# Optimization experiments

Measured on AMD Instinct MI355X. Metric: run time of the kernel, lower is better.

Reference implementation:

```python
import jax, jax.numpy as jnp
import numpy as np

N = 100000   # nodes
E = 1600000  # directed edges (avg degree 16)
H = 64       # MODEL_HIDDEN_CHANNELS


def setup_inputs() -> dict:
    key = jax.random.key(0)
    ks = jax.random.split(key, 6)
    x = jax.random.normal(ks[0], (N, 1), dtype=jnp.float32)
    edge_index = jax.random.randint(ks[1], (2, E), 0, N, dtype=jnp.int32)
    w1 = jax.random.normal(ks[2], (1, H), dtype=jnp.float32) * 0.5
    b1 = jnp.zeros((H,), dtype=jnp.float32)
    w2 = jax.random.normal(ks[3], (H, H), dtype=jnp.float32) * (1.0 / np.sqrt(H))
    b2 = jnp.zeros((H,), dtype=jnp.float32)
    wfc = jax.random.normal(ks[4], (H, 1), dtype=jnp.float32) * (1.0 / np.sqrt(H))
    bfc = jnp.zeros((1,), dtype=jnp.float32)
    return {"x": x, "edge_index": edge_index, "w1": w1, "b1": b1,
            "w2": w2, "b2": b2, "wfc": wfc, "bfc": bfc}


def _gcn_conv(x, src, dst, norm, W, b, n):
    # PyG GCNConv: h = x @ W, then scatter-add of norm-weighted messages at dst, + bias
    h = x @ W                                   # [n, out]
    msg = h[src] * norm[:, None]                # gather + scale, [e, out]
    agg = jax.ops.segment_sum(msg, dst, num_segments=n)
    return agg + b


def reference(x, edge_index, w1, b1, w2, b2, wfc, bfc):
    n = x.shape[0]
    # add self-loops (PyG GCNConv default)
    loops = jnp.arange(n, dtype=edge_index.dtype)
    src = jnp.concatenate([edge_index[0], loops])
    dst = jnp.concatenate([edge_index[1], loops])
    # symmetric degree normalization D^{-1/2} A_hat D^{-1/2}
    deg = jax.ops.segment_sum(jnp.ones(src.shape[0], dtype=x.dtype), dst, num_segments=n)
    dinv = jnp.where(deg > 0, jax.lax.rsqrt(deg), 0.0)
    norm = dinv[src] * dinv[dst]
    h = jax.nn.relu(_gcn_conv(x, src, dst, norm, w1, b1, n))
    h = jax.nn.relu(_gcn_conv(h, src, dst, norm, w2, b2, n))
    out = h @ wfc + bfc                         # [n, 1]
    return out.reshape(-1)
```

## Files before the change

kernel.cpp:

```cpp
#include <hip/hip_runtime.h>


#define HCH 64
#define CHUNK 4096
#define BSH 8
#define BSZ 256
#define NBMAX 512

__device__ __forceinline__ void lds_addf(float* p, float v) {
    __hip_atomic_fetch_add(p, v, __ATOMIC_RELAXED, __HIP_MEMORY_SCOPE_WORKGROUP);
}

__global__ __launch_bounds__(512) void k_init(int nb, int cap,
                                              int* __restrict__ cursor,
                                              int* __restrict__ ov_cursor,
                                              const float* __restrict__ w1,
                                              const float* __restrict__ b1,
                                              const float* __restrict__ w2,
                                              float* __restrict__ P) {
    __shared__ float part[8][4][HCH];
    int t = threadIdx.x;
    for (int i = t; i < nb; i += 512) cursor[i] = i * cap;
    if (t == 0) *ov_cursor = 0;
    int j = t & 63, seg = t >> 6;
    float pp = 0.f, pm = 0.f, bp = 0.f, bm = 0.f;
#pragma unroll
    for (int kk = 0; kk < 8; kk++) {
        int k = seg * 8 + kk;
        float w = w1[k], b = b1[k], v = w2[k * HCH + j];
        if (w > 0.f) { pp += w * v; bp += b * v; }
        else if (w < 0.f) { pm += w * v; bm += b * v; }
        else { float rb = b > 0.f ? b : 0.f; bp += rb * v; bm += rb * v; }
    }
    part[seg][0][j] = pp; part[seg][1][j] = pm;
    part[seg][2][j] = bp; part[seg][3][j] = bm;
    __syncthreads();
    if (t < 4 * HCH) {
        int c = t >> 6, jj = t & 63;
        float s = 0.f;
#pragma unroll
        for (int g = 0; g < 8; g++) s += part[g][c][jj];
        P[c * HCH + jj] = s;
    }
}

__global__ __launch_bounds__(256) void k_place(const int* __restrict__ src,
                                               const int* __restrict__ dst, int e,
                                               int nb, int cap,
                                               int* __restrict__ cursor,
                                               int* __restrict__ ov_cursor,
                                               int* __restrict__ packed,
                                               int2* __restrict__ ovbuf) {
    __shared__ int h[NBMAX];
    __shared__ int basel[NBMAX];
    __shared__ int avail[NBMAX];
    int t = threadIdx.x;
    for (int i = t; i < nb; i += 256) h[i] = 0;
    __syncthreads();
    int cbase = blockIdx.x * CHUNK;
    int cend = min(e, cbase + CHUNK);
    for (int i = cbase + t; i < cend; i += 256) atomicAdd(&h[dst[i] >> BSH], 1);
    __syncthreads();
    for (int i = t; i < nb; i += 256) {
        int my = h[i];
        int av = 0, base = 0;
        if (my) {
            base = atomicAdd(&cursor[i], my);
            int room = (i + 1) * cap - base;
            av = room < 0 ? 0 : (room > my ? my : room);
        }
        basel[i] = base;
        avail[i] = av;
        h[i] = 0;
    }
    __syncthreads();
    for (int i = cbase + t; i < cend; i += 256) {
        int d = dst[i], sv = src[i];
        int b = d >> BSH;
        int loc = atomicAdd(&h[b], 1);
        if (loc < avail[b]) {
            packed[basel[b] + loc] = sv | ((d & (BSZ - 1)) << 17);
        } else {
            int op = atomicAdd(ov_cursor, 1);
            ovbuf[op] = make_int2(sv, d);
        }
    }
}

__global__ __launch_bounds__(512) void k_bdeg(const int* __restrict__ packed,
                                              const int* __restrict__ cursor,
                                              const int* __restrict__ ov_cursor,
                                              const int2* __restrict__ ovbuf,
                                              int cap, const float* __restrict__ x, int n,
                                              float* __restrict__ dinv,
                                              float* __restrict__ y) {
    __shared__ int cnt[BSZ];
    int bk = blockIdx.x, t = threadIdx.x;
    int bbase = bk * cap;
    int bcnt = min(cursor[bk] - bbase, cap);
    if (t < BSZ) cnt[t] = 0;
    __syncthreads();
    for (int i = t; i < bcnt; i += 512) atomicAdd(&cnt[packed[bbase + i] >> 17], 1);
    int ovc = *ov_cursor;
    for (int i = t; i < ovc; i += 512) {
        int2 o = ovbuf[i];
        if ((o.y >> BSH) == bk) atomicAdd(&cnt[o.y & (BSZ - 1)], 1);
    }
    __syncthreads();
    int node = (bk << BSH) + t;
    if (t < BSZ && node < n) {
        float dv = rsqrtf((float)(cnt[t] + 1));
        dinv[node] = dv;
        y[node] = dv * x[node];
    }
}

__global__ __launch_bounds__(512) void k_bagg1(const int* __restrict__ packed,
                                               const int* __restrict__ cursor,
                                               const int* __restrict__ ov_cursor,
                                               const int2* __restrict__ ovbuf,
                                               int cap, const float* __restrict__ x,
                                               const float* __restrict__ dinv,
                                               const float* __restrict__ y, int n,
                                               float2* __restrict__ val2) {
    __shared__ float acc[BSZ];
    int bk = blockIdx.x, t = threadIdx.x;
    int bbase = bk * cap;
    int bcnt = min(cursor[bk] - bbase, cap);
    if (t < BSZ) acc[t] = 0.f;
    __syncthreads();
    for (int i = t; i < bcnt; i += 512) {
        int p = packed[bbase + i];
        lds_addf(&acc[p >> 17], y[p & 0x1FFFF]);
    }
    int ovc = *ov_cursor;
    for (int i = t; i < ovc; i += 512) {
        int2 o = ovbuf[i];
        if ((o.y >> BSH) == bk) lds_addf(&acc[o.y & (BSZ - 1)], y[o.x]);
    }
    __syncthreads();
    int node = (bk << BSH) + t;
    if (t < BSZ && node < n) {
        float dv = dinv[node];
        float s = dv * (acc[t] + dv * x[node]);
        val2[node] = make_float2(dv * s, dv);
    }
}

__global__ __launch_bounds__(512) void k_bagg2(const int* __restrict__ packed,
                                               const int* __restrict__ cursor,
                                               const int* __restrict__ ov_cursor,
                                               const int2* __restrict__ ovbuf,
                                               int cap, const float2* __restrict__ val2,
                                               const float* __restrict__ dinv,
                                               const float* __restrict__ P,
                                               const float* __restrict__ b2,
                                               const float* __restrict__ wfc,
                                               const float* __restrict__ bfc,
                                               float* __restrict__ out, int n) {
    __shared__ float ap[BSZ], am[BSZ], cp[BSZ], cm[BSZ];
    __shared__ float sP[4 * HCH], sb2[HCH], swfc[HCH];
    int bk = blockIdx.x, t = threadIdx.x;
    int bbase = bk * cap;
    int bcnt = min(cursor[bk] - bbase, cap);
    if (t < BSZ) { ap[t] = 0.f; am[t] = 0.f; cp[t] = 0.f; cm[t] = 0.f; }
    if (t < 4 * HCH) sP[t] = P[t];
    if (t >= 4 * HCH && t < 5 * HCH) sb2[t - 4 * HCH] = b2[t - 4 * HCH];
    if (t >= 5 * HCH && t < 6 * HCH) swfc[t - 5 * HCH] = wfc[t - 5 * HCH];
    __syncthreads();
    for (int i = t; i < bcnt; i += 512) {
        int p = packed[bbase + i];
        int ld = p >> 17;
        float2 v = val2[p & 0x1FFFF];
        if (v.x > 0.f) { lds_addf(&ap[ld], v.x); lds_addf(&cp[ld], v.y); }
        else           { lds_addf(&am[ld], v.x); lds_addf(&cm[ld], v.y); }
    }
    int ovc = *ov_cursor;
    for (int i = t; i < ovc; i += 512) {
        int2 o = ovbuf[i];
        if ((o.y >> BSH) == bk) {
            int ld = o.y & (BSZ - 1);
            float2 v = val2[o.x];
            if (v.x > 0.f) { lds_addf(&ap[ld], v.x); lds_addf(&cp[ld], v.y); }
            else           { lds_addf(&am[ld], v.x); lds_addf(&cm[ld], v.y); }
        }
    }
    __syncthreads();
    int node = (bk << BSH) + t;
    if (t >= BSZ || node >= n) return;
    float a_p = ap[t], a_m = am[t], c_p = cp[t], c_m = cm[t];
    float2 sv = val2[node];
    if (sv.x > 0.f) { a_p += sv.x; c_p += sv.y; }
    else            { a_m += sv.x; c_m += sv.y; }
    float dv = dinv[node];
    float acc = 0.f;
#pragma unroll 8
    for (int j = 0; j < HCH; j++) {
        float z = dv * (a_p * sP[j] + a_m * sP[HCH + j] +
                        c_p * sP[2 * HCH + j] + c_m * sP[3 * HCH + j]) + sb2[j];
        z = z > 0.f ? z : 0.f;
        acc += z * swfc[j];
    }
    out[node] = acc + bfc[0];
}

extern "C" void kernel_launch(void* const* d_in, const int* in_sizes, int n_in,
                              void* d_out, int out_size, void* d_ws, size_t ws_size,
                              hipStream_t stream) {
    const float* x   = (const float*)d_in[0];
    const int*   ei  = (const int*)d_in[1];
    const float* w1  = (const float*)d_in[2];
    const float* b1  = (const float*)d_in[3];
    const float* w2  = (const float*)d_in[4];
    const float* b2  = (const float*)d_in[5];
    const float* wfc = (const float*)d_in[6];
    const float* bfc = (const float*)d_in[7];
    float* out = (float*)d_out;

    const int n = in_sizes[0];
    const int e = in_sizes[1] / 2;
    const int* src = ei;
    const int* dst = ei + e;

    const int nb = (n + BSZ - 1) >> BSH;
    int avg = (e + nb - 1) / nb;
    int cap = avg + avg / 4 + 64;

    auto al = [](size_t v) { return (v + 255) & ~(size_t)255; };
    char* ws = (char*)d_ws;
    size_t o = 0;
    int* cursor    = (int*)(ws + o);  o = al(o + (size_t)NBMAX * 4);
    int* ov_cursor = (int*)(ws + o);  o = al(o + 256);
    float* dinv  = (float*)(ws + o);  o = al(o + (size_t)n * 4);
    float* y     = (float*)(ws + o);  o = al(o + (size_t)n * 4);
    float2* val2 = (float2*)(ws + o); o = al(o + (size_t)n * 8);
    float* P     = (float*)(ws + o);  o = al(o + 4 * HCH * 4);
    int* packed  = (int*)(ws + o);    o = al(o + (size_t)nb * cap * 4);
    int2* ovbuf  = (int2*)(ws + o);   o = al(o + (size_t)e * 8);
    (void)ws_size;

    const int nchunk = (e + CHUNK - 1) / CHUNK;

    k_init<<<1, 512, 0, stream>>>(nb, cap, cursor, ov_cursor, w1, b1, w2, P);
    k_place<<<nchunk, 256, 0, stream>>>(src, dst, e, nb, cap, cursor, ov_cursor,
                                        packed, ovbuf);
    k_bdeg<<<nb, 512, 0, stream>>>(packed, cursor, ov_cursor, ovbuf, cap, x, n, dinv, y);
    k_bagg1<<<nb, 512, 0, stream>>>(packed, cursor, ov_cursor, ovbuf, cap, x, dinv, y,
                                    n, val2);
    k_bagg2<<<nb, 512, 0, stream>>>(packed, cursor, ov_cursor, ovbuf, cap, val2, dinv,
                                    P, b2, wfc, bfc, out, n);
}
```

Baseline: 147.9 us.

## Halve bucket size, stage edges in LDS, vectorise packed loads, skip zero-bias accumulation

```diff
diff --git a/kernel.cpp b/kernel.cpp
--- a/kernel.cpp
+++ b/kernel.cpp
@@ -3,9 +3,9 @@
 
 #define HCH 64
 #define CHUNK 4096
-#define BSH 8
-#define BSZ 256
-#define NBMAX 512
+#define BSH 7
+#define BSZ 128
+#define NBMAX 1024
 
 __device__ __forceinline__ void lds_addf(float* p, float v) {
     __hip_atomic_fetch_add(p, v, __ATOMIC_RELAXED, __HIP_MEMORY_SCOPE_WORKGROUP);
@@ -19,9 +19,11 @@
                                               const float* __restrict__ w2,
                                               float* __restrict__ P) {
     __shared__ float part[8][4][HCH];
+    __shared__ float sPo[4 * HCH];
+    __shared__ float fsum;
     int t = threadIdx.x;
     for (int i = t; i < nb; i += 512) cursor[i] = i * cap;
-    if (t == 0) *ov_cursor = 0;
+    if (t == 0) { *ov_cursor = 0; fsum = 0.f; }
     int j = t & 63, seg = t >> 6;
     float pp = 0.f, pm = 0.f, bp = 0.f, bm = 0.f;
 #pragma unroll
@@ -40,11 +42,15 @@
         float s = 0.f;
 #pragma unroll
         for (int g = 0; g < 8; g++) s += part[g][c][jj];
-        P[c * HCH + jj] = s;
-    }
-}
-
-__global__ __launch_bounds__(256) void k_place(const int* __restrict__ src,
+        sPo[t] = s;
+        P[t] = s;
+        if (c >= 2) lds_addf(&fsum, fabsf(s));
+    }
+    __syncthreads();
+    if (t == 0) P[4 * HCH] = fsum;
+}
+
+__global__ __launch_bounds__(512) void k_place(const int* __restrict__ src,
                                                const int* __restrict__ dst, int e,
                                                int nb, int cap,
                                                int* __restrict__ cursor,
@@ -54,14 +60,40 @@
     __shared__ int h[NBMAX];
     __shared__ int basel[NBMAX];
     __shared__ int avail[NBMAX];
+    __shared__ int lpv[CHUNK];
+    __shared__ short lb[CHUNK];
     int t = threadIdx.x;
-    for (int i = t; i < nb; i += 256) h[i] = 0;
+    for (int i = t; i < nb; i += 512) h[i] = 0;
     __syncthreads();
     int cbase = blockIdx.x * CHUNK;
-    int cend = min(e, cbase + CHUNK);
-    for (int i = cbase + t; i < cend; i += 256) atomicAdd(&h[dst[i] >> BSH], 1);
-    __syncthreads();
-    for (int i = t; i < nb; i += 256) {
+    int rem = min(e - cbase, CHUNK);
+#pragma unroll
+    for (int g = 0; g < 2; g++) {
+        int li = t * 8 + g * 4;
+        if (li + 3 < rem) {
+            int4 s4 = *(const int4*)(src + cbase + li);
+            int4 d4 = *(const int4*)(dst + cbase + li);
+#pragma unroll
+            for (int q = 0; q < 4; q++) {
+                int sv = (q == 0) ? s4.x : (q == 1) ? s4.y : (q == 2) ? s4.z : s4.w;
+                int dv = (q == 0) ? d4.x : (q == 1) ? d4.y : (q == 2) ? d4.z : d4.w;
+                int b = dv >> BSH;
+                atomicAdd(&h[b], 1);
+                lpv[li + q] = sv | ((dv & (BSZ - 1)) << 17);
+                lb[li + q] = (short)b;
+            }
+        } else {
+            for (int q = li; q < rem && q < li + 4; q++) {
+                int sv = src[cbase + q], dv = dst[cbase + q];
+                int b = dv >> BSH;
+                atomicAdd(&h[b], 1);
+                lpv[q] = sv | ((dv & (BSZ - 1)) << 17);
+                lb[q] = (short)b;
+            }
+        }
+    }
+    __syncthreads();
+    for (int i = t; i < nb; i += 512) {
         int my = h[i];
         int av = 0, base = 0;
         if (my) {
@@ -74,15 +106,15 @@
         h[i] = 0;
     }
     __syncthreads();
-    for (int i = cbase + t; i < cend; i += 256) {
-        int d = dst[i], sv = src[i];
-        int b = d >> BSH;
+    for (int li = t * 8; li < t * 8 + 8 && li < rem; li++) {
+        int b = lb[li];
+        int pv = lpv[li];
         int loc = atomicAdd(&h[b], 1);
         if (loc < avail[b]) {
-            packed[basel[b] + loc] = sv | ((d & (BSZ - 1)) << 17);
+            packed[basel[b] + loc] = pv;
         } else {
             int op = atomicAdd(ov_cursor, 1);
-            ovbuf[op] = make_int2(sv, d);
+            ovbuf[op] = make_int2(pv & 0x1FFFF, (b << BSH) | (pv >> 17));
         }
     }
 }
@@ -100,7 +132,19 @@
     int bcnt = min(cursor[bk] - bbase, cap);
     if (t < BSZ) cnt[t] = 0;
     __syncthreads();
-    for (int i = t; i < bcnt; i += 512) atomicAdd(&cnt[packed[bbase + i] >> 17], 1);
+    for (int base = 0; base < bcnt; base += 2048) {
+        int i0 = base + t * 4;
+        if (i0 + 3 < bcnt) {
+            int4 p = *(const int4*)(packed + bbase + i0);
+            atomicAdd(&cnt[p.x >> 17], 1);
+            atomicAdd(&cnt[p.y >> 17], 1);
+            atomicAdd(&cnt[p.z >> 17], 1);
+            atomicAdd(&cnt[p.w >> 17], 1);
+        } else {
+            for (int i = i0; i < bcnt && i < i0 + 4; i++)
+                atomicAdd(&cnt[packed[bbase + i] >> 17], 1);
+        }
+    }
     int ovc = *ov_cursor;
     for (int i = t; i < ovc; i += 512) {
         int2 o = ovbuf[i];
@@ -129,9 +173,22 @@
     int bcnt = min(cursor[bk] - bbase, cap);
     if (t < BSZ) acc[t] = 0.f;
     __syncthreads();
-    for (int i = t; i < bcnt; i += 512) {
-        int p = packed[bbase + i];
-        lds_addf(&acc[p >> 17], y[p & 0x1FFFF]);
+    for (int base = 0; base < bcnt; base += 2048) {
+        int i0 = base + t * 4;
+        if (i0 + 3 < bcnt) {
+            int4 p = *(const int4*)(packed + bbase + i0);
+            float y0 = y[p.x & 0x1FFFF], y1 = y[p.y & 0x1FFFF];
+            float y2 = y[p.z & 0x1FFFF], y3 = y[p.w & 0x1FFFF];
+            lds_addf(&acc[p.x >> 17], y0);
+            lds_addf(&acc[p.y >> 17], y1);
+            lds_addf(&acc[p.z >> 17], y2);
+            lds_addf(&acc[p.w >> 17], y3);
+        } else {
+            for (int i = i0; i < bcnt && i < i0 + 4; i++) {
+                int p = packed[bbase + i];
+                lds_addf(&acc[p >> 17], y[p & 0x1FFFF]);
+            }
+        }
     }
     int ovc = *ov_cursor;
     for (int i = t; i < ovc; i += 512) {
@@ -158,37 +215,60 @@
                                                const float* __restrict__ wfc,
                                                const float* __restrict__ bfc,
                                                float* __restrict__ out, int n) {
-    __shared__ float ap[BSZ], am[BSZ], cp[BSZ], cm[BSZ];
+    __shared__ float aa[2 * BSZ];
+    __shared__ float cc[2 * BSZ];
     __shared__ float sP[4 * HCH], sb2[HCH], swfc[HCH];
+    __shared__ float sflag;
     int bk = blockIdx.x, t = threadIdx.x;
     int bbase = bk * cap;
     int bcnt = min(cursor[bk] - bbase, cap);
-    if (t < BSZ) { ap[t] = 0.f; am[t] = 0.f; cp[t] = 0.f; cm[t] = 0.f; }
+    if (t < 2 * BSZ) { aa[t] = 0.f; cc[t] = 0.f; }
     if (t < 4 * HCH) sP[t] = P[t];
-    if (t >= 4 * HCH && t < 5 * HCH) sb2[t - 4 * HCH] = b2[t - 4 * HCH];
-    if (t >= 5 * HCH && t < 6 * HCH) swfc[t - 5 * HCH] = wfc[t - 5 * HCH];
-    __syncthreads();
-    for (int i = t; i < bcnt; i += 512) {
-        int p = packed[bbase + i];
-        int ld = p >> 17;
-        float2 v = val2[p & 0x1FFFF];
-        if (v.x > 0.f) { lds_addf(&ap[ld], v.x); lds_addf(&cp[ld], v.y); }
-        else           { lds_addf(&am[ld], v.x); lds_addf(&cm[ld], v.y); }
+    if (t >= 256 && t < 320) sb2[t - 256] = b2[t - 256];
+    if (t >= 320 && t < 384) swfc[t - 320] = wfc[t - 320];
+    if (t == 448) sflag = P[4 * HCH];
+    __syncthreads();
+    bool useB = sflag != 0.f;
+    for (int base = 0; base < bcnt; base += 2048) {
+        int i0 = base + t * 4;
+        if (i0 + 3 < bcnt) {
+            int4 p = *(const int4*)(packed + bbase + i0);
+            float2 v0 = val2[p.x & 0x1FFFF], v1 = val2[p.y & 0x1FFFF];
+            float2 v2 = val2[p.z & 0x1FFFF], v3 = val2[p.w & 0x1FFFF];
+            int o0 = (v0.x > 0.f ? 0 : BSZ) + (p.x >> 17);
+            int o1 = (v1.x > 0.f ? 0 : BSZ) + (p.y >> 17);
+            int o2 = (v2.x > 0.f ? 0 : BSZ) + (p.z >> 17);
+            int o3 = (v3.x > 0.f ? 0 : BSZ) + (p.w >> 17);
+            lds_addf(&aa[o0], v0.x); lds_addf(&aa[o1], v1.x);
+            lds_addf(&aa[o2], v2.x); lds_addf(&aa[o3], v3.x);
+            if (useB) {
+                lds_addf(&cc[o0], v0.y); lds_addf(&cc[o1], v1.y);
+                lds_addf(&cc[o2], v2.y); lds_addf(&cc[o3], v3.y);
+            }
+        } else {
+            for (int i = i0; i < bcnt && i < i0 + 4; i++) {
+                int p = packed[bbase + i];
+                float2 v = val2[p & 0x1FFFF];
+                int off = (v.x > 0.f ? 0 : BSZ) + (p >> 17);
+                lds_addf(&aa[off], v.x);
+                if (useB) lds_addf(&cc[off], v.y);
+            }
+        }
     }
     int ovc = *ov_cursor;
     for (int i = t; i < ovc; i += 512) {
         int2 o = ovbuf[i];
         if ((o.y >> BSH) == bk) {
-            int ld = o.y & (BSZ - 1);
             float2 v = val2[o.x];
-            if (v.x > 0.f) { lds_addf(&ap[ld], v.x); lds_addf(&cp[ld], v.y); }
-            else           { lds_addf(&am[ld], v.x); lds_addf(&cm[ld], v.y); }
+            int off = (v.x > 0.f ? 0 : BSZ) + (o.y & (BSZ - 1));
+            lds_addf(&aa[off], v.x);
+            if (useB) lds_addf(&cc[off], v.y);
         }
     }
     __syncthreads();
     int node = (bk << BSH) + t;
     if (t >= BSZ || node >= n) return;
-    float a_p = ap[t], a_m = am[t], c_p = cp[t], c_m = cm[t];
+    float a_p = aa[t], a_m = aa[BSZ + t], c_p = cc[t], c_m = cc[BSZ + t];
     float2 sv = val2[node];
     if (sv.x > 0.f) { a_p += sv.x; c_p += sv.y; }
     else            { a_m += sv.x; c_m += sv.y; }
@@ -224,7 +304,7 @@
 
     const int nb = (n + BSZ - 1) >> BSH;
     int avg = (e + nb - 1) / nb;
-    int cap = avg + avg / 4 + 64;
+    int cap = ((avg + avg / 4 + 64) + 15) & ~15;
 
     auto al = [](size_t v) { return (v + 255) & ~(size_t)255; };
     char* ws = (char*)d_ws;
@@ -234,7 +314,7 @@
     float* dinv  = (float*)(ws + o);  o = al(o + (size_t)n * 4);
     float* y     = (float*)(ws + o);  o = al(o + (size_t)n * 4);
     float2* val2 = (float2*)(ws + o); o = al(o + (size_t)n * 8);
-    float* P     = (float*)(ws + o);  o = al(o + 4 * HCH * 4);
+    float* P     = (float*)(ws + o);  o = al(o + (4 * HCH + 8) * 4);
     int* packed  = (int*)(ws + o);    o = al(o + (size_t)nb * cap * 4);
     int2* ovbuf  = (int2*)(ws + o);   o = al(o + (size_t)e * 8);
     (void)ws_size;
@@ -242,7 +322,7 @@
     const int nchunk = (e + CHUNK - 1) / CHUNK;
 
     k_init<<<1, 512, 0, stream>>>(nb, cap, cursor, ov_cursor, w1, b1, w2, P);
-    k_place<<<nchunk, 256, 0, stream>>>(src, dst, e, nb, cap, cursor, ov_cursor,
+    k_place<<<nchunk, 512, 0, stream>>>(src, dst, e, nb, cap, cursor, ov_cursor,
                                         packed, ovbuf);
     k_bdeg<<<nb, 512, 0, stream>>>(packed, cursor, ov_cursor, ovbuf, cap, x, n, dinv, y);
     k_bagg1<<<nb, 512, 0, stream>>>(packed, cursor, ov_cursor, ovbuf, cap, x, dinv, y,
```

After: 134.5 us. -9.1%, faster.
